# Optimization experiments

Measured on AMD Instinct MI355X. Metric: run time of the kernel, lower is better.

## Reference

```python
import jax, jax.numpy as jnp
import numpy as np

HIDDEN = 1024
NUM_HEADS = 16
HEAD_DIM = HIDDEN // NUM_HEADS


def setup_inputs() -> dict:
    key = jax.random.key(0)
    ks = jax.random.split(key, 9)
    s = 0.02
    return {
        "x": jax.random.normal(ks[0], (2, 2048, HIDDEN), dtype=jnp.float32),
        "wq": jax.random.normal(ks[1], (HIDDEN, HIDDEN), dtype=jnp.float32) * s,
        "bq": jnp.zeros((HIDDEN,), dtype=jnp.float32),
        "wk": jax.random.normal(ks[2], (HIDDEN, HIDDEN), dtype=jnp.float32) * s,
        "bk": jnp.zeros((HIDDEN,), dtype=jnp.float32),
        "wv": jax.random.normal(ks[3], (HIDDEN, HIDDEN), dtype=jnp.float32) * s,
        "bv": jnp.zeros((HIDDEN,), dtype=jnp.float32),
        "wo": jax.random.normal(ks[4], (HIDDEN, HIDDEN), dtype=jnp.float32) * s,
        "bo": jnp.zeros((HIDDEN,), dtype=jnp.float32),
    }


def reference(x, wq, bq, wk, bk, wv, bv, wo, bo):
    B, S, H = x.shape
    # torch nn.Linear: y = x @ W.T + b
    q = x @ wq.T + bq
    k = x @ wk.T + bk
    v = x @ wv.T + bv
    # [B, S, nH, dH] -> [B, nH, S, dH]
    q = q.reshape(B, S, NUM_HEADS, HEAD_DIM).transpose(0, 2, 1, 3)
    k = k.reshape(B, S, NUM_HEADS, HEAD_DIM).transpose(0, 2, 1, 3)
    v = v.reshape(B, S, NUM_HEADS, HEAD_DIM).transpose(0, 2, 1, 3)
    scores = jnp.einsum("bhqd,bhkd->bhqk", q, k)
    probs = jax.nn.softmax(scores / jnp.sqrt(jnp.float32(HEAD_DIM)), axis=-1)
    context = jnp.einsum("bhqk,bhkd->bhqd", probs, v)
    context = context.transpose(0, 2, 1, 3).reshape(B, S, H)
    return context @ wo.T + bo
```

## Files before the change

### kernel.cpp

```cpp
#include <hip/hip_runtime.h>
#include <hip/hip_bf16.h>
#include <math.h>

#define HID   1024
#define NHEAD 16
#define DHEAD 64
#define BATCH 2
#define SEQ   2048
#define TOK   (BATCH*SEQ)

#define LOG2E_8 0.18033688011112042f

typedef float f32x4  __attribute__((ext_vector_type(4)));
typedef short short8 __attribute__((ext_vector_type(8)));

__device__ __forceinline__ unsigned short f2bf(float f) {
    unsigned int u = __float_as_uint(f);
    u += 0x7FFFu + ((u >> 16) & 1u);
    return (unsigned short)(u >> 16);
}

__device__ __forceinline__ unsigned pk2(float lo, float hi) {
    union { __hip_bfloat162 h; unsigned u; } cv;
    cv.h = __float22bfloat162_rn(make_float2(lo, hi));
    return cv.u;
}

__device__ __forceinline__ float fexp2(float x) {
#if __has_builtin(__builtin_amdgcn_exp2f)
    return __builtin_amdgcn_exp2f(x);
#else
    return __expf(x * 0.6931471805599453f);
#endif
}

__device__ __forceinline__ void gll16(const unsigned short* g, unsigned short* l) {
    __builtin_amdgcn_global_load_lds(
        (const __attribute__((address_space(1))) void*)g,
        (__attribute__((address_space(3))) void*)l, 16, 0, 0);
}

__global__ __launch_bounds__(256) void cvt_all(
    const float* __restrict__ x,  const float* __restrict__ wq,
    const float* __restrict__ wk, const float* __restrict__ wv,
    const float* __restrict__ wo,
    unsigned short* __restrict__ xb,  unsigned short* __restrict__ wqb,
    unsigned short* __restrict__ wkb, unsigned short* __restrict__ wvb,
    unsigned short* __restrict__ wob, int nx, int nw)
{
    const int i = blockIdx.x * 256 + threadIdx.x;
    const int z = blockIdx.y;
    const float* in; unsigned short* out; int n; float s = 1.0f;
    switch (z) {
        case 0:  in = x;  out = xb;  n = nx; break;
        case 1:  in = wq; out = wqb; n = nw; s = LOG2E_8; break;
        case 2:  in = wk; out = wkb; n = nw; break;
        case 3:  in = wv; out = wvb; n = nw; break;
        default: in = wo; out = wob; n = nw; break;
    }
    if (i >= n) return;
    const float4* p = (const float4*)in;
    float4 a = p[2*i], b = p[2*i+1];
    uint4 r;
    r.x = pk2(a.x*s, a.y*s); r.y = pk2(a.z*s, a.w*s);
    r.z = pk2(b.x*s, b.y*s); r.w = pk2(b.z*s, b.w*s);
    ((uint4*)out)[i] = r;
}

template<int BM, int BN, int NZ, bool OUTF32, int MINW>
__global__ __launch_bounds__(256, MINW) void gemm_t(
    const unsigned short* __restrict__ A,
    const unsigned short* __restrict__ W0, const unsigned short* __restrict__ W1,
    const unsigned short* __restrict__ W2,
    const float* __restrict__ b0, const float* __restrict__ b1, const float* __restrict__ b2,
    void* __restrict__ C0, void* __restrict__ C1, void* __restrict__ C2,
    int M, int N, int K)
{
    constexpr int MT = BM/32;
    constexpr int NT = BN/32;
    constexpr int AG = BM/64;
    constexpr int WG = BN/64;

    __shared__ unsigned short As[BM*32];
    __shared__ unsigned short Ws[BN*32];

    const unsigned short* W = W0; const float* bias = b0; void* C = C0;
    int z = 0;
    if (NZ > 1) {
        z = blockIdx.z;
        W    = (z==0) ? W0 : ((z==1) ? W1 : W2);
        bias = (z==0) ? b0 : ((z==1) ? b1 : b2);
        C    = (z==0) ? C0 : ((z==1) ? C1 : C2);
    }
    const int tid  = threadIdx.x;
    const int l15  = tid & 15, quad = (tid >> 4) & 3, w = tid >> 6;
    const int wm   = (w >> 1) * (BM/2), wn = (w & 1) * (BN/2);
    const int m0   = blockIdx.y * BM, n0 = blockIdx.x * BN;

    const int lane = tid & 63;
    const int grow = lane >> 2;
    const int gchk = (lane & 3) ^ (grow & 3);

    const unsigned short* pA[AG]; unsigned short* lA[AG];
    const unsigned short* pW[WG]; unsigned short* lW[WG];
    #pragma unroll
    for (int i = 0; i < AG; ++i) {
        const int r = w*(BM/4) + i*16;
        pA[i] = A + (size_t)(m0 + r + grow) * K + gchk*8;
        lA[i] = &As[r * 32];
    }
    #pragma unroll
    for (int i = 0; i < WG; ++i) {
        const int r = w*(BN/4) + i*16;
        pW[i] = W + (size_t)(n0 + r + grow) * K + gchk*8;
        lW[i] = &Ws[r * 32];
    }

    f32x4 acc[MT][NT] = {};

    for (int k0 = 0; k0 < K; k0 += 32) {
        #pragma unroll
        for (int i = 0; i < AG; ++i) { gll16(pA[i], lA[i]); pA[i] += 32; }
        #pragma unroll
        for (int i = 0; i < WG; ++i) { gll16(pW[i], lW[i]); pW[i] += 32; }
        __syncthreads();

        const int co = (quad ^ (l15 & 3)) * 8;
        short8 af[MT], bfv[NT];
        #pragma unroll
        for (int mi = 0; mi < MT; ++mi) af[mi]  = *(const short8*)&As[(wm + mi*16 + l15)*32 + co];
        #pragma unroll
        for (int ni = 0; ni < NT; ++ni) bfv[ni] = *(const short8*)&Ws[(wn + ni*16 + l15)*32 + co];
        #pragma unroll
        for (int mi = 0; mi < MT; ++mi)
            #pragma unroll
            for (int ni = 0; ni < NT; ++ni)
                acc[mi][ni] = __builtin_amdgcn_mfma_f32_16x16x32_bf16(af[mi], bfv[ni], acc[mi][ni], 0, 0, 0);
        __syncthreads();
    }

    const float bsc = (NZ == 3 && z == 0) ? LOG2E_8 : 1.0f;
    float bv[NT];
    #pragma unroll
    for (int ni = 0; ni < NT; ++ni) bv[ni] = bias[n0 + wn + ni*16 + l15] * bsc;

    if (NZ == 3 && z == 2) {
        #pragma unroll
        for (int mi = 0; mi < MT; ++mi)
            #pragma unroll
            for (int ni = 0; ni < NT; ++ni) {
                const int row0 = m0 + wm + mi*16 + quad*4;
                const int col  = n0 + wn + ni*16 + l15;
                const int hh = col >> 6, dd = col & 63;
                const int bb = row0 >> 11, ss = row0 & 2047;
                ushort4 r4;
                r4.x = f2bf(acc[mi][ni][0] + bv[ni]);
                r4.y = f2bf(acc[mi][ni][1] + bv[ni]);
                r4.z = f2bf(acc[mi][ni][2] + bv[ni]);
                r4.w = f2bf(acc[mi][ni][3] + bv[ni]);
                *(ushort4*)((unsigned short*)C + ((size_t)(bb*NHEAD + hh)*DHEAD + dd)*SEQ + ss) = r4;
            }
    } else {
        #pragma unroll
        for (int mi = 0; mi < MT; ++mi)
            #pragma unroll
            for (int ni = 0; ni < NT; ++ni)
                #pragma unroll
                for (int r = 0; r < 4; ++r) {
                    const int row = m0 + wm + mi*16 + quad*4 + r;
                    const int col = n0 + wn + ni*16 + l15;
                    const float val = acc[mi][ni][r] + bv[ni];
                    if (OUTF32) ((float*)C)[(size_t)row*N + col] = val;
                    else ((unsigned short*)C)[(size_t)row*N + col] = f2bf(val);
                }
    }
}

__global__ __launch_bounds__(256, 3) void attn_v6(
    const unsigned short* __restrict__ Qg, const unsigned short* __restrict__ Kg,
    const unsigned short* __restrict__ vT,
    unsigned short* __restrict__ pO0, unsigned short* __restrict__ pO1,
    unsigned short* __restrict__ pO2, unsigned short* __restrict__ pO3,
    float* __restrict__ pl)
{
    __shared__ unsigned short Ks[32][64];
    __shared__ unsigned short VT[64][32];
    __shared__ unsigned short PT[4][64][32];

    const int tid  = threadIdx.x;
    const int l15  = tid & 15, quad = (tid >> 4) & 3, w = tid >> 6;
    const int z    = blockIdx.z;
    const int b    = z & 1, half = z >> 1;
    const int h    = blockIdx.y;
    const int q0   = blockIdx.x * 256;
    const size_t rowbase = (size_t)b * SEQ;
    const int    cbase   = h * DHEAD;
    const size_t vbase   = (size_t)(b*NHEAD + h) * DHEAD * SEQ;
    const int    keybase = half * (SEQ/4);

    short8 qa[4][2];
    #pragma unroll
    for (int nq = 0; nq < 4; ++nq)
        #pragma unroll
        for (int s2 = 0; s2 < 2; ++s2)
            qa[nq][s2] = *(const short8*)(Qg + (rowbase + q0 + w*64 + nq*16 + l15) * HID
                                             + cbase + s2*32 + quad*8);

    const int kr_ = tid >> 3, kc_ = tid & 7;
    const int ksc = kc_ ^ (kr_ & 7);
    const int vd_ = tid >> 2, vkc = tid & 3;
    const int vsc = vkc ^ ((vd_ >> 1) & 3);
    const unsigned short* kgp = Kg + (rowbase + keybase + kr_) * HID + cbase + kc_*8;
    const unsigned short* vgp = vT + vbase + (size_t)vd_ * SEQ + keybase + vkc*8;

    f32x4 o[4][4] = {};
    float lsum[4] = {0.f, 0.f, 0.f, 0.f};
    const int fsw = (l15 >> 1) & 3;

    for (int kt = 0; kt < SEQ/4/32; ++kt) {
        const uint4 kv4 = *(const uint4*)kgp;  kgp += (size_t)32 * HID;
        const uint4 vv4 = *(const uint4*)vgp;  vgp += 32;
        __syncthreads();
        *(uint4*)&Ks[kr_][ksc*8] = kv4;
        *(uint4*)&VT[vd_][vsc*8] = vv4;
        __syncthreads();

        f32x4 s[2][4] = {};
        #pragma unroll
        for (int s2 = 0; s2 < 2; ++s2) {
            short8 kf[2];
            #pragma unroll
            for (int mi = 0; mi < 2; ++mi)
                kf[mi] = *(const short8*)&Ks[mi*16 + l15][((((s2<<2)|quad)) ^ (l15 & 7)) * 8];
            #pragma unroll
            for (int mi = 0; mi < 2; ++mi)
                #pragma unroll
                for (int nq = 0; nq < 4; ++nq)
                    s[mi][nq] = __builtin_amdgcn_mfma_f32_16x16x32_bf16(kf[mi], qa[nq][s2], s[mi][nq], 0, 0, 0);
        }

        #pragma unroll
        for (int mi = 0; mi < 2; ++mi)
            #pragma unroll
            for (int nq = 0; nq < 4; ++nq) {
                const float p0 = fexp2(s[mi][nq][0]);
                const float p1 = fexp2(s[mi][nq][1]);
                const float p2 = fexp2(s[mi][nq][2]);
                const float p3 = fexp2(s[mi][nq][3]);
                lsum[nq] += (p0 + p1) + (p2 + p3);
                uint2 u; u.x = pk2(p0, p1); u.y = pk2(p2, p3);
                const int sc = (2*mi + (quad >> 1)) ^ fsw;
                *(uint2*)&PT[w][nq*16 + l15][sc*8 + (quad & 1)*4] = u;
            }

        short8 ptb[4], vf[4];
        #pragma unroll
        for (int nq = 0; nq < 4; ++nq)
            ptb[nq] = *(const short8*)&PT[w][nq*16 + l15][(quad ^ fsw) * 8];
        #pragma unroll
        for (int md = 0; md < 4; ++md)
            vf[md] = *(const short8*)&VT[md*16 + l15][(quad ^ fsw) * 8];
        #pragma unroll
        for (int md = 0; md < 4; ++md)
            #pragma unroll
            for (int nq = 0; nq < 4; ++nq)
                o[md][nq] = __builtin_amdgcn_mfma_f32_16x16x32_bf16(vf[md], ptb[nq], o[md][nq], 0, 0, 0);
    }

    unsigned short* pO = (half == 0) ? pO0 : ((half == 1) ? pO1 : ((half == 2) ? pO2 : pO3));
    #pragma unroll
    for (int nq = 0; nq < 4; ++nq) {
        float l = lsum[nq];
        l += __shfl_xor(l, 16);
        l += __shfl_xor(l, 32);
        if (quad == 0)
            pl[(((size_t)half * BATCH + b) * NHEAD + h) * SEQ + q0 + w*64 + nq*16 + l15] = l;
        const size_t row = rowbase + q0 + w*64 + nq*16 + l15;
        #pragma unroll
        for (int md = 0; md < 4; ++md) {
            ushort4 u;
            u.x = f2bf(o[md][nq][0]); u.y = f2bf(o[md][nq][1]);
            u.z = f2bf(o[md][nq][2]); u.w = f2bf(o[md][nq][3]);
            *(ushort4*)&pO[row * HID + cbase + md*16 + quad*4] = u;
        }
    }
}

__device__ __forceinline__ unsigned addquad(unsigned a, unsigned b, unsigned c,
                                            unsigned d, float inv) {
    const float s0 = __uint_as_float(a << 16) + __uint_as_float(b << 16)
                   + __uint_as_float(c << 16) + __uint_as_float(d << 16);
    const float s1 = __uint_as_float(a & 0xffff0000u) + __uint_as_float(b & 0xffff0000u)
                   + __uint_as_float(c & 0xffff0000u) + __uint_as_float(d & 0xffff0000u);
    return pk2(s0 * inv, s1 * inv);
}

__global__ __launch_bounds__(256) void reduce4(
    const unsigned short* __restrict__ p0, const unsigned short* __restrict__ p1,
    const unsigned short* __restrict__ p2, const unsigned short* __restrict__ p3,
    const float* __restrict__ pl, unsigned short* __restrict__ ctx)
{
    const int i  = blockIdx.x * 256 + threadIdx.x;
    const int e0 = i * 8;
    const int t  = e0 >> 10;
    const int h  = (e0 & 1023) >> 6;
    const int b  = t >> 11, q = t & 2047;
    const size_t lb = ((size_t)b * NHEAD + h) * SEQ + q;
    const size_t lstep = (size_t)BATCH * NHEAD * SEQ;
    const float l = pl[lb] + pl[lb + lstep] + pl[lb + 2*lstep] + pl[lb + 3*lstep];
    const float inv = 1.f / l;
    uint4 a = ((const uint4*)p0)[i];
    uint4 b4 = ((const uint4*)p1)[i];
    uint4 c = ((const uint4*)p2)[i];
    uint4 d = ((const uint4*)p3)[i];
    uint4 r;
    r.x = addquad(a.x, b4.x, c.x, d.x, inv);
    r.y = addquad(a.y, b4.y, c.y, d.y, inv);
    r.z = addquad(a.z, b4.z, c.z, d.z, inv);
    r.w = addquad(a.w, b4.w, c.w, d.w, inv);
    ((uint4*)ctx)[i] = r;
}

extern "C" void kernel_launch(void* const* d_in, const int* in_sizes, int n_in,
                              void* d_out, int out_size, void* d_ws, size_t ws_size,
                              hipStream_t stream)
{
    const float* x  = (const float*)d_in[0];
    const float* wq = (const float*)d_in[1];
    const float* bq = (const float*)d_in[2];
    const float* wk = (const float*)d_in[3];
    const float* bk = (const float*)d_in[4];
    const float* wv = (const float*)d_in[5];
    const float* bv = (const float*)d_in[6];
    const float* wo = (const float*)d_in[7];
    const float* bo = (const float*)d_in[8];
    float* out = (float*)d_out;

    unsigned short* xb  = (unsigned short*)d_ws;
    unsigned short* wqb = xb  + (size_t)TOK * HID;
    unsigned short* wkb = wqb + (size_t)HID * HID;
    unsigned short* wvb = wkb + (size_t)HID * HID;
    unsigned short* wob = wvb + (size_t)HID * HID;
    unsigned short* qb  = wob + (size_t)HID * HID;
    unsigned short* kb  = qb  + (size_t)TOK * HID;
    unsigned short* vtb = kb  + (size_t)TOK * HID;
    unsigned short* cb  = vtb + (size_t)TOK * HID;
    unsigned short* cb2 = cb  + (size_t)TOK * HID;
    unsigned short* cb3 = cb2 + (size_t)TOK * HID;

    const dim3 blk(256);

    cvt_all<<<dim3(TOK*HID/8/256, 5), blk, 0, stream>>>(
        x, wq, wk, wv, wo, xb, wqb, wkb, wvb, wob, TOK*HID/8, HID*HID/8);

    gemm_t<128, 128, 3, false, 3><<<dim3(HID/128, TOK/128, 3), blk, 0, stream>>>(
        xb, wqb, wkb, wvb, bq, bk, bv, qb, kb, vtb, TOK, HID, HID);

    attn_v6<<<dim3(SEQ/256, NHEAD, BATCH*4), blk, 0, stream>>>(
        qb, kb, vtb, xb, cb, cb2, cb3, (float*)wqb);

    reduce4<<<dim3(TOK*HID/8/256), blk, 0, stream>>>(
        xb, cb, cb2, cb3, (float*)wqb, qb);

    gemm_t<128, 64, 1, true, 4><<<dim3(HID/64, TOK/128, 1), blk, 0, stream>>>(
        qb, wob, wob, wob, bo, bo, bo, out, out, out, TOK, HID, HID);
}
```

Measured before the change: 205.3 us.

## Double-buffer K/V tiles in attention kernel with register prefetch

Adds double-buffered shared memory for the K and V tiles. The next tile is prefetched into registers while the current one is computed, then stored into the alternate buffer after the MFMAs, which removes one __syncthreads per iteration and hides global load latency. Launch bounds rise from 3 to 4 blocks per CU, which tightens the register budget. The extra shared memory and the live prefetch registers could raise register pressure or cause spills.

```diff
diff --git a/kernel.cpp b/kernel.cpp
--- a/kernel.cpp
+++ b/kernel.cpp
@@ -176,15 +176,15 @@
     }
 }
 
-__global__ __launch_bounds__(256, 3) void attn_v6(
+__global__ __launch_bounds__(256, 4) void attn_v7(
     const unsigned short* __restrict__ Qg, const unsigned short* __restrict__ Kg,
     const unsigned short* __restrict__ vT,
     unsigned short* __restrict__ pO0, unsigned short* __restrict__ pO1,
     unsigned short* __restrict__ pO2, unsigned short* __restrict__ pO3,
     float* __restrict__ pl)
 {
-    __shared__ unsigned short Ks[32][64];
-    __shared__ unsigned short VT[64][32];
+    __shared__ unsigned short Ks[2][32][64];
+    __shared__ unsigned short VT[2][64][32];
     __shared__ unsigned short PT[4][64][32];
 
     const int tid  = threadIdx.x;
@@ -213,17 +213,27 @@
     const unsigned short* kgp = Kg + (rowbase + keybase + kr_) * HID + cbase + kc_*8;
     const unsigned short* vgp = vT + vbase + (size_t)vd_ * SEQ + keybase + vkc*8;
 
+    {
+        const uint4 k0 = *(const uint4*)kgp;  kgp += (size_t)32 * HID;
+        const uint4 v0 = *(const uint4*)vgp;  vgp += 32;
+        *(uint4*)&Ks[0][kr_][ksc*8] = k0;
+        *(uint4*)&VT[0][vd_][vsc*8] = v0;
+    }
+
     f32x4 o[4][4] = {};
     float lsum[4] = {0.f, 0.f, 0.f, 0.f};
     const int fsw = (l15 >> 1) & 3;
 
     for (int kt = 0; kt < SEQ/4/32; ++kt) {
-        const uint4 kv4 = *(const uint4*)kgp;  kgp += (size_t)32 * HID;
-        const uint4 vv4 = *(const uint4*)vgp;  vgp += 32;
+        const int buf = kt & 1;
         __syncthreads();
-        *(uint4*)&Ks[kr_][ksc*8] = kv4;
-        *(uint4*)&VT[vd_][vsc*8] = vv4;
-        __syncthreads();
+
+        uint4 kn, vn;
+        const bool pre = (kt + 1 < SEQ/4/32);
+        if (pre) {
+            kn = *(const uint4*)kgp;  kgp += (size_t)32 * HID;
+            vn = *(const uint4*)vgp;  vgp += 32;
+        }
 
         f32x4 s[2][4] = {};
         #pragma unroll
@@ -231,7 +241,7 @@
             short8 kf[2];
             #pragma unroll
             for (int mi = 0; mi < 2; ++mi)
-                kf[mi] = *(const short8*)&Ks[mi*16 + l15][((((s2<<2)|quad)) ^ (l15 & 7)) * 8];
+                kf[mi] = *(const short8*)&Ks[buf][mi*16 + l15][((((s2<<2)|quad)) ^ (l15 & 7)) * 8];
             #pragma unroll
             for (int mi = 0; mi < 2; ++mi)
                 #pragma unroll
@@ -259,12 +269,18 @@
             ptb[nq] = *(const short8*)&PT[w][nq*16 + l15][(quad ^ fsw) * 8];
         #pragma unroll
         for (int md = 0; md < 4; ++md)
-            vf[md] = *(const short8*)&VT[md*16 + l15][(quad ^ fsw) * 8];
+            vf[md] = *(const short8*)&VT[buf][md*16 + l15][(quad ^ fsw) * 8];
         #pragma unroll
         for (int md = 0; md < 4; ++md)
             #pragma unroll
             for (int nq = 0; nq < 4; ++nq)
                 o[md][nq] = __builtin_amdgcn_mfma_f32_16x16x32_bf16(vf[md], ptb[nq], o[md][nq], 0, 0, 0);
+
+        if (pre) {
+            const int nb = buf ^ 1;
+            *(uint4*)&Ks[nb][kr_][ksc*8] = kn;
+            *(uint4*)&VT[nb][vd_][vsc*8] = vn;
+        }
     }
 
     unsigned short* pO = (half == 0) ? pO0 : ((half == 1) ? pO1 : ((half == 2) ? pO2 : pO3));
@@ -356,7 +372,7 @@
     gemm_t<128, 128, 3, false, 3><<<dim3(HID/128, TOK/128, 3), blk, 0, stream>>>(
         xb, wqb, wkb, wvb, bq, bk, bv, qb, kb, vtb, TOK, HID, HID);
 
-    attn_v6<<<dim3(SEQ/256, NHEAD, BATCH*4), blk, 0, stream>>>(
+    attn_v7<<<dim3(SEQ/256, NHEAD, BATCH*4), blk, 0, stream>>>(
         qb, kb, vtb, xb, cb, cb2, cb3, (float*)wqb);
 
     reduce4<<<dim3(TOK*HID/8/256), blk, 0, stream>>>(
```

Result: slower. 339.9 us (+65.6%).
